# Kernel tuning notes

Hardware: AMD Instinct MI355X
Metric: run time of the kernel (lower is better)

## Reference

```python
import jax, jax.numpy as jnp
import numpy as np

N, E, D, K = 32768, 16384, 4, 8          # nodes, hyperedges, edges/node, nodes/edge
IN_DIM, OUT_DIM, EDGE_DIM, NUM_HEADS = 128, 128, 64, 8


def setup_inputs() -> dict:
    key = jax.random.key(0)
    ks = jax.random.split(key, 16)
    s_in = 1.0 / np.sqrt(IN_DIM)
    s_out = 1.0 / np.sqrt(OUT_DIM)
    s_edge = 1.0 / np.sqrt(EDGE_DIM)
    return {
        "x": jax.random.normal(ks[0], (N, IN_DIM), jnp.float32),
        "edge_attr": jax.random.normal(ks[1], (E, EDGE_DIM), jnp.float32),
        "node_edges": jax.random.randint(ks[2], (N, D), 0, E),   # hyperedges containing each node
        "edge_nodes": jax.random.randint(ks[3], (E, K), 0, N),   # nodes inside each hyperedge
        "W_lin": jax.random.normal(ks[4], (OUT_DIM, IN_DIM), jnp.float32) * s_in,
        "W_edge": jax.random.normal(ks[5], (OUT_DIM, EDGE_DIM), jnp.float32) * s_edge,
        "Wq": jax.random.normal(ks[6], (OUT_DIM, OUT_DIM), jnp.float32) * s_out,
        "Wk": jax.random.normal(ks[7], (OUT_DIM, OUT_DIM), jnp.float32) * s_out,
        "Wv": jax.random.normal(ks[8], (OUT_DIM, OUT_DIM), jnp.float32) * s_out,
        "bq": jnp.zeros((OUT_DIM,), jnp.float32),
        "bk": jnp.zeros((OUT_DIM,), jnp.float32),
        "bv": jnp.zeros((OUT_DIM,), jnp.float32),
        "Wo": jax.random.normal(ks[9], (OUT_DIM, OUT_DIM), jnp.float32) * s_out,
        "bo": jnp.zeros((OUT_DIM,), jnp.float32),
    }


def reference(x, edge_attr, node_edges, edge_nodes,
              W_lin, W_edge, Wq, Wk, Wv, bq, bk, bv, Wo, bo):
    n, out_dim = x.shape[0], W_lin.shape[0]
    hd = out_dim // NUM_HEADS
    L = node_edges.shape[1] * edge_nodes.shape[1]  # D*K keys per node

    Wh = x @ W_lin.T                               # [N, out]
    We = edge_attr @ W_edge.T                      # [E, out]

    u_idx = edge_nodes[node_edges]                 # [N, D, K] neighbor node ids
    vals = Wh[u_idx]                               # [N, D, K, out]
    keys = vals + We[node_edges][:, :, None, :]    # key = Wh[u] + We[e]
    keys = keys.reshape(n, L, out_dim)
    vals = vals.reshape(n, L, out_dim)

    # torch nn.MultiheadAttention: single query per node (query = Wh[v])
    q = (Wh @ Wq.T + bq).reshape(n, NUM_HEADS, hd)
    k = (keys @ Wk.T + bk).reshape(n, L, NUM_HEADS, hd)
    v = (vals @ Wv.T + bv).reshape(n, L, NUM_HEADS, hd)

    scores = jnp.einsum('nhd,nlhd->nhl', q, k) / jnp.sqrt(jnp.asarray(hd, q.dtype))
    attn = jax.nn.softmax(scores, axis=-1)         # [N, H, L]
    ctx = jnp.einsum('nhl,nlhd->nhd', attn, v).reshape(n, out_dim)
    out = ctx @ Wo.T + bo
    return jax.nn.relu(out)
```

## Files before the change

kernel.cpp:

```cpp
#include <hip/hip_runtime.h>

#define N_NODES 32768
#define N_EDGES 16384
#define DEG 4
#define KPE 8
#define DIM 128
#define EDIM 64

typedef float f32x4 __attribute__((ext_vector_type(4)));
typedef __bf16 bf16x8 __attribute__((ext_vector_type(8)));
typedef __bf16 bf16x2 __attribute__((ext_vector_type(2)));
typedef unsigned short u16x8 __attribute__((ext_vector_type(8)));
typedef unsigned int u32;
typedef unsigned int u32x4 __attribute__((ext_vector_type(4)));
typedef int i32x4 __attribute__((ext_vector_type(4)));

static __device__ __forceinline__ unsigned short f2bf(float f) {
  union { float f; unsigned int u; } v; v.f = f;
  unsigned int r = (v.u + 0x7FFFu + ((v.u >> 16) & 1u)) >> 16;
  return (unsigned short)r;
}
static __device__ __forceinline__ float bflo(unsigned int v) {
  union { unsigned int u; float f; } x; x.u = v << 16; return x.f;
}
static __device__ __forceinline__ float bfhi(unsigned int v) {
  union { unsigned int u; float f; } x; x.u = v & 0xffff0000u; return x.f;
}

#if __has_builtin(__builtin_amdgcn_fdot2_f32_bf16)
static __device__ __forceinline__ float dot2bf(unsigned int a, unsigned int b, float c) {
  return __builtin_amdgcn_fdot2_f32_bf16(
      __builtin_bit_cast(bf16x2, a), __builtin_bit_cast(bf16x2, b), c, false);
}
#else
static __device__ __forceinline__ float dot2bf(unsigned int a, unsigned int b, float c) {
  c = fmaf(bflo(a), bflo(b), c);
  return fmaf(bfhi(a), bfhi(b), c);
}
#endif

__global__ __launch_bounds__(256) void wprep_kernel(
    const float* __restrict__ Wq, const float* __restrict__ Wk,
    const float* __restrict__ Wv, const float* __restrict__ Wlin,
    const float* __restrict__ Wedge, const float* __restrict__ Wo,
    const int* __restrict__ node_edges, const int* __restrict__ enodes,
    unsigned short* __restrict__ CW, unsigned short* __restrict__ CWE,
    unsigned short* __restrict__ Wob, int* __restrict__ uidx)
{
  int id = blockIdx.x * 256 + threadIdx.x;
  if (id < 384 * 128) {
    int j = id >> 7, i = id & 127;
    const float* wrow; float scale = 1.0f;
    if (j < 128)      { wrow = Wq + j * 128; scale = 0.25f; }
    else if (j < 256) { wrow = Wk + (j - 128) * 128; }
    else              { wrow = Wv + (j - 256) * 128; }
    float s = 0.f;
    #pragma unroll 8
    for (int m = 0; m < 128; ++m) s += wrow[m] * Wlin[m * 128 + i];
    CW[id] = f2bf(s * scale);
  } else if (id < 384 * 128 + 128 * 64) {
    int id2 = id - 384 * 128; int j = id2 >> 6, t = id2 & 63;
    float s = 0.f;
    #pragma unroll 8
    for (int m = 0; m < 128; ++m) s += Wk[j * 128 + m] * Wedge[m * 64 + t];
    CWE[id2] = f2bf(s);
  } else if (id < 384 * 128 + 128 * 64 + 128 * 128) {
    int id3 = id - (384 * 128 + 128 * 64);
    Wob[id3] = f2bf(Wo[id3]);
  } else {
    int t = id - (384 * 128 + 128 * 64 + 128 * 128);
    int e = node_edges[t];
    i32x4 a = *(const i32x4*)(enodes + (size_t)e * KPE);
    i32x4 b = *(const i32x4*)(enodes + (size_t)e * KPE + 4);
    *(i32x4*)(uidx + (size_t)t * KPE)     = a;
    *(i32x4*)(uidx + (size_t)t * KPE + 4) = b;
  }
}

__global__ __launch_bounds__(256) void g12_kernel(
    const float* __restrict__ x, const unsigned short* __restrict__ CW,
    const float* __restrict__ bq, const float* __restrict__ bv,
    unsigned short* __restrict__ qb, unsigned short* __restrict__ Kb,
    unsigned short* __restrict__ Vb,
    const float* __restrict__ ea, const unsigned short* __restrict__ CWE,
    const float* __restrict__ bk, unsigned short* __restrict__ WeKb)
{
  const int wave = threadIdx.x >> 6, lane = threadIdx.x & 63;
  const int r16 = lane & 15, quad = lane >> 4;

  if (blockIdx.x < 512) {
    const int m0 = blockIdx.x * 64 + wave * 16;
    u16x8 av[4];
    const float* arow = x + (size_t)(m0 + r16) * DIM + quad * 8;
    #pragma unroll
    for (int kk = 0; kk < 4; ++kk) {
      float4 a0 = *(const float4*)(arow + kk * 32);
      float4 a1 = *(const float4*)(arow + kk * 32 + 4);
      u16x8 au;
      au[0] = f2bf(a0.x); au[1] = f2bf(a0.y); au[2] = f2bf(a0.z); au[3] = f2bf(a0.w);
      au[4] = f2bf(a1.x); au[5] = f2bf(a1.y); au[6] = f2bf(a1.z); au[7] = f2bf(a1.w);
      av[kk] = au;
    }
    #pragma unroll
    for (int g = 0; g < 6; ++g) {
      f32x4 acc[4];
      const f32x4 z = {0.f, 0.f, 0.f, 0.f};
      acc[0] = z; acc[1] = z; acc[2] = z; acc[3] = z;
      #pragma unroll
      for (int kk = 0; kk < 4; ++kk) {
        #pragma unroll
        for (int s = 0; s < 4; ++s) {
          u16x8 bu = *(const u16x8*)(CW + (size_t)(g * 64 + s * 16 + r16) * DIM + kk * 32 + quad * 8);
          acc[s] = __builtin_amdgcn_mfma_f32_16x16x32_bf16(
              __builtin_bit_cast(bf16x8, av[kk]), __builtin_bit_cast(bf16x8, bu), acc[s], 0, 0, 0);
        }
      }
      const int arr = g >> 1;
      const int colbase = (g & 1) * 64;
      unsigned short* dst = arr == 0 ? qb : (arr == 1 ? Kb : Vb);
      #pragma unroll
      for (int s = 0; s < 4; ++s) {
        int j = colbase + s * 16 + r16;
        float bias = arr == 0 ? 0.25f * bq[j] : (arr == 2 ? bv[j] : 0.f);
        #pragma unroll
        for (int r = 0; r < 4; ++r) {
          int m = m0 + quad * 4 + r;
          dst[(size_t)m * DIM + j] = f2bf(acc[s][r] + bias);
        }
      }
    }
  } else {
    const int idx = blockIdx.x - 512;
    const int m0 = (idx >> 1) * 64 + wave * 16;
    const int n0 = (idx & 1) * 64;
    f32x4 acc[4];
    const f32x4 z = {0.f, 0.f, 0.f, 0.f};
    acc[0] = z; acc[1] = z; acc[2] = z; acc[3] = z;
    const float* arow = ea + (size_t)(m0 + r16) * EDIM + quad * 8;
    #pragma unroll
    for (int kk = 0; kk < 2; ++kk) {
      float4 a0 = *(const float4*)(arow + kk * 32);
      float4 a1 = *(const float4*)(arow + kk * 32 + 4);
      u16x8 au;
      au[0] = f2bf(a0.x); au[1] = f2bf(a0.y); au[2] = f2bf(a0.z); au[3] = f2bf(a0.w);
      au[4] = f2bf(a1.x); au[5] = f2bf(a1.y); au[6] = f2bf(a1.z); au[7] = f2bf(a1.w);
      bf16x8 av = __builtin_bit_cast(bf16x8, au);
      #pragma unroll
      for (int s = 0; s < 4; ++s) {
        u16x8 bu = *(const u16x8*)(CWE + (size_t)(n0 + s * 16 + r16) * EDIM + kk * 32 + quad * 8);
        acc[s] = __builtin_amdgcn_mfma_f32_16x16x32_bf16(
            av, __builtin_bit_cast(bf16x8, bu), acc[s], 0, 0, 0);
      }
    }
    #pragma unroll
    for (int s = 0; s < 4; ++s) {
      int j = n0 + s * 16 + r16;
      float bias = bk[j];
      #pragma unroll
      for (int r = 0; r < 4; ++r) {
        int m = m0 + quad * 4 + r;
        WeKb[(size_t)m * DIM + j] = f2bf(acc[s][r] + bias);
      }
    }
  }
}

__global__ __launch_bounds__(64, 4) void attn_kernel(
    const unsigned short* __restrict__ qb, const unsigned short* __restrict__ Kb,
    const unsigned short* __restrict__ Vb, const unsigned short* __restrict__ WeKb,
    const int* __restrict__ nedges, const int* __restrict__ uidx,
    unsigned short* __restrict__ ctxb)
{
  __shared__ __align__(16) unsigned char ldsK[32 * 272];
  __shared__ __align__(16) unsigned char ldsE[4 * 272];
  __shared__ __align__(16) float ldsP[8][36];
  const int lane = threadIdx.x;
  const int n = blockIdx.x;
  const int l = lane & 31, half = lane >> 5;
  const int h = lane >> 3;
  const int c0 = lane * 2;

  const i32x4* up = (const i32x4*)(uidx + (size_t)n * 32);
  i32x4 m0 = __builtin_nontemporal_load(up + 0);
  i32x4 m1 = __builtin_nontemporal_load(up + 1);
  i32x4 m2 = __builtin_nontemporal_load(up + 2);
  i32x4 m3 = __builtin_nontemporal_load(up + 3);
  i32x4 m4 = __builtin_nontemporal_load(up + 4);
  i32x4 m5 = __builtin_nontemporal_load(up + 5);
  i32x4 m6 = __builtin_nontemporal_load(up + 6);
  i32x4 m7 = __builtin_nontemporal_load(up + 7);
  i32x4 e4 = __builtin_nontemporal_load((const i32x4*)(nedges + (size_t)n * DEG));

  const u32x4* qp = (const u32x4*)(qb + (size_t)n * DIM + half * 64);
  u32x4 qv[8];
  #pragma unroll
  for (int ch = 0; ch < 8; ++ch) qv[ch] = __builtin_nontemporal_load(qp + ch);

  asm volatile("" ::: "memory");

#define STAGE(ldsdst, table, row) do {                                          \
    const u32* gp_ = (const u32*)((table) + (size_t)(row) * DIM) + lane;        \
    __builtin_amdgcn_global_load_lds(                                           \
        (const __attribute__((address_space(1))) u32*)gp_,                      \
        (__attribute__((address_space(3))) u32*)(ldsdst), 4, 0, 0);             \
  } while (0)
  STAGE(ldsK + 0  * 272, Kb, m0.x); STAGE(ldsK + 1  * 272, Kb, m0.y);
  STAGE(ldsK + 2  * 272, Kb, m0.z); STAGE(ldsK + 3  * 272, Kb, m0.w);
  STAGE(ldsK + 4  * 272, Kb, m1.x); STAGE(ldsK + 5  * 272, Kb, m1.y);
  STAGE(ldsK + 6  * 272, Kb, m1.z); STAGE(ldsK + 7  * 272, Kb, m1.w);
  STAGE(ldsK + 8  * 272, Kb, m2.x); STAGE(ldsK + 9  * 272, Kb, m2.y);
  STAGE(ldsK + 10 * 272, Kb, m2.z); STAGE(ldsK + 11 * 272, Kb, m2.w);
  STAGE(ldsK + 12 * 272, Kb, m3.x); STAGE(ldsK + 13 * 272, Kb, m3.y);
  STAGE(ldsK + 14 * 272, Kb, m3.z); STAGE(ldsK + 15 * 272, Kb, m3.w);
  STAGE(ldsK + 16 * 272, Kb, m4.x); STAGE(ldsK + 17 * 272, Kb, m4.y);
  STAGE(ldsK + 18 * 272, Kb, m4.z); STAGE(ldsK + 19 * 272, Kb, m4.w);
  STAGE(ldsK + 20 * 272, Kb, m5.x); STAGE(ldsK + 21 * 272, Kb, m5.y);
  STAGE(ldsK + 22 * 272, Kb, m5.z); STAGE(ldsK + 23 * 272, Kb, m5.w);
  STAGE(ldsK + 24 * 272, Kb, m6.x); STAGE(ldsK + 25 * 272, Kb, m6.y);
  STAGE(ldsK + 26 * 272, Kb, m6.z); STAGE(ldsK + 27 * 272, Kb, m6.w);
  STAGE(ldsK + 28 * 272, Kb, m7.x); STAGE(ldsK + 29 * 272, Kb, m7.y);
  STAGE(ldsK + 30 * 272, Kb, m7.z); STAGE(ldsK + 31 * 272, Kb, m7.w);
  STAGE(ldsE + 0 * 272, WeKb, e4.x); STAGE(ldsE + 1 * 272, WeKb, e4.y);
  STAGE(ldsE + 2 * 272, WeKb, e4.z); STAGE(ldsE + 3 * 272, WeKb, e4.w);
#undef STAGE

  asm volatile("" ::: "memory");

  u32 vv[32];
#define VLOAD(t, row) vv[t] = *(const u32*)(Vb + (size_t)(row) * DIM + c0)
  VLOAD(0,  m0.x); VLOAD(1,  m0.y); VLOAD(2,  m0.z); VLOAD(3,  m0.w);
  VLOAD(4,  m1.x); VLOAD(5,  m1.y); VLOAD(6,  m1.z); VLOAD(7,  m1.w);
  VLOAD(8,  m2.x); VLOAD(9,  m2.y); VLOAD(10, m2.z); VLOAD(11, m2.w);
  VLOAD(12, m3.x); VLOAD(13, m3.y); VLOAD(14, m3.z); VLOAD(15, m3.w);
  VLOAD(16, m4.x); VLOAD(17, m4.y); VLOAD(18, m4.z); VLOAD(19, m4.w);
  VLOAD(20, m5.x); VLOAD(21, m5.y); VLOAD(22, m5.z); VLOAD(23, m5.w);
  VLOAD(24, m6.x); VLOAD(25, m6.y); VLOAD(26, m6.z); VLOAD(27, m6.w);
  VLOAD(28, m7.x); VLOAD(29, m7.y); VLOAD(30, m7.z); VLOAD(31, m7.w);
#undef VLOAD

  asm volatile("s_waitcnt vmcnt(32)" ::: "memory");

  const unsigned char* krow = ldsK + l * 272 + half * 128;
  const unsigned char* erow = ldsE + (l >> 3) * 272 + half * 128;
  float s[4] = {0.f, 0.f, 0.f, 0.f};
  #pragma unroll
  for (int ch = 0; ch < 8; ++ch) {
    uint4 kc = *(const uint4*)(krow + ch * 16);
    uint4 ec = *(const uint4*)(erow + ch * 16);
    const int hi = ch >> 1;
    float t = s[hi];
    t = dot2bf(qv[ch].x, kc.x, t); t = dot2bf(qv[ch].x, ec.x, t);
    t = dot2bf(qv[ch].y, kc.y, t); t = dot2bf(qv[ch].y, ec.y, t);
    t = dot2bf(qv[ch].z, kc.z, t); t = dot2bf(qv[ch].z, ec.z, t);
    t = dot2bf(qv[ch].w, kc.w, t); t = dot2bf(qv[ch].w, ec.w, t);
    s[hi] = t;
  }

  #pragma unroll
  for (int hi = 0; hi < 4; ++hi) {
    float vmax = s[hi];
    #pragma unroll
    for (int off = 16; off >= 1; off >>= 1)
      vmax = fmaxf(vmax, __shfl_xor(vmax, off, 32));
    float ex = __expf(s[hi] - vmax);
    float sum = ex;
    #pragma unroll
    for (int off = 16; off >= 1; off >>= 1)
      sum += __shfl_xor(sum, off, 32);
    ldsP[half * 4 + hi][l] = ex / sum;
  }

  float a0 = 0.f, a1 = 0.f;
  #pragma unroll
  for (int t = 0; t < 8; ++t) {
    float4 p4 = *(const float4*)&ldsP[h][t * 4];
    a0 = fmaf(p4.x, bflo(vv[t * 4 + 0]), a0); a1 = fmaf(p4.x, bfhi(vv[t * 4 + 0]), a1);
    a0 = fmaf(p4.y, bflo(vv[t * 4 + 1]), a0); a1 = fmaf(p4.y, bfhi(vv[t * 4 + 1]), a1);
    a0 = fmaf(p4.z, bflo(vv[t * 4 + 2]), a0); a1 = fmaf(p4.z, bfhi(vv[t * 4 + 2]), a1);
    a0 = fmaf(p4.w, bflo(vv[t * 4 + 3]), a0); a1 = fmaf(p4.w, bfhi(vv[t * 4 + 3]), a1);
  }
  unsigned int pk = (unsigned int)f2bf(a0) | ((unsigned int)f2bf(a1) << 16);
  __builtin_nontemporal_store(pk, (u32*)(ctxb + (size_t)n * DIM + c0));
}

__global__ __launch_bounds__(256) void g4_kernel(
    const unsigned short* __restrict__ ctxb, const unsigned short* __restrict__ Wob,
    const float* __restrict__ bo, float* __restrict__ out)
{
  const int wave = threadIdx.x >> 6, lane = threadIdx.x & 63;
  const int r16 = lane & 15, quad = lane >> 4;
  const int m0 = blockIdx.x * 64 + wave * 16;
  const int n0 = blockIdx.y * 64;

  f32x4 acc[4];
  const f32x4 z = {0.f, 0.f, 0.f, 0.f};
  acc[0] = z; acc[1] = z; acc[2] = z; acc[3] = z;

  #pragma unroll
  for (int kk = 0; kk < 4; ++kk) {
    u16x8 au = *(const u16x8*)(ctxb + (size_t)(m0 + r16) * DIM + kk * 32 + quad * 8);
    bf16x8 av = __builtin_bit_cast(bf16x8, au);
    #pragma unroll
    for (int s = 0; s < 4; ++s) {
      u16x8 bu = *(const u16x8*)(Wob + (size_t)(n0 + s * 16 + r16) * DIM + kk * 32 + quad * 8);
      acc[s] = __builtin_amdgcn_mfma_f32_16x16x32_bf16(
          av, __builtin_bit_cast(bf16x8, bu), acc[s], 0, 0, 0);
    }
  }

  #pragma unroll
  for (int s = 0; s < 4; ++s) {
    int j = n0 + s * 16 + r16;
    float bias = bo[j];
    #pragma unroll
    for (int r = 0; r < 4; ++r) {
      int m = m0 + quad * 4 + r;
      float v = acc[s][r] + bias;
      out[(size_t)m * DIM + j] = v > 0.f ? v : 0.f;
    }
  }
}

extern "C" void kernel_launch(void* const* d_in, const int* in_sizes, int n_in,
                              void* d_out, int out_size, void* d_ws, size_t ws_size,
                              hipStream_t stream)
{
  const float* x     = (const float*)d_in[0];
  const float* ea    = (const float*)d_in[1];
  const int* nedges  = (const int*)d_in[2];
  const int* enodes  = (const int*)d_in[3];
  const float* Wlin  = (const float*)d_in[4];
  const float* Wedge = (const float*)d_in[5];
  const float* Wq    = (const float*)d_in[6];
  const float* Wk    = (const float*)d_in[7];
  const float* Wv    = (const float*)d_in[8];
  const float* bq    = (const float*)d_in[9];
  const float* bk    = (const float*)d_in[10];
  const float* bv    = (const float*)d_in[11];
  const float* Wo    = (const float*)d_in[12];
  const float* bo    = (const float*)d_in[13];
  float* out = (float*)d_out;

  unsigned short* wsp = (unsigned short*)d_ws;
  unsigned short* CW   = wsp;  wsp += 384 * 128;
  unsigned short* CWE  = wsp;  wsp += 128 * 64;
  unsigned short* Wob  = wsp;  wsp += 128 * 128;
  unsigned short* qb   = wsp;  wsp += (size_t)N_NODES * DIM;
  unsigned short* Kb   = wsp;  wsp += (size_t)N_NODES * DIM;
  unsigned short* Vb   = wsp;  wsp += (size_t)N_NODES * DIM;
  unsigned short* WeKb = wsp;  wsp += (size_t)N_EDGES * DIM;
  unsigned short* ctxb = wsp;  wsp += (size_t)N_NODES * DIM;
  int* uidx = (int*)wsp;       wsp += (size_t)N_NODES * 32 * 2;

  wprep_kernel<<<dim3(800), dim3(256), 0, stream>>>(
      Wq, Wk, Wv, Wlin, Wedge, Wo, nedges, enodes, CW, CWE, Wob, uidx);
  g12_kernel<<<dim3(1024), dim3(256), 0, stream>>>(x, CW, bq, bv, qb, Kb, Vb, ea, CWE, bk, WeKb);
  attn_kernel<<<dim3(32768), dim3(64), 0, stream>>>(qb, Kb, Vb, WeKb, nedges, uidx, ctxb);
  g4_kernel<<<dim3(512, 2), dim3(256), 0, stream>>>(ctxb, Wob, bo, out);
}
```

Before: 205.2 us.

## Process two nodes per attention block with double-buffered LDS gather pipelining

Each attention workgroup now handles two nodes and double-buffers the K/edge LDS staging. The second node's index loads, K gathers and V loads are issued while the first node's scores and context are computed. The aim is to hide gather latency inside a single wave rather than relying only on occupancy. In exchange the block uses twice the LDS and more registers, the launch bound drops to 2 waves per SIMD, and the hand-tuned vmcnt counts must exactly match the issued loads.

```diff
diff --git a/kernel.cpp b/kernel.cpp
--- a/kernel.cpp
+++ b/kernel.cpp
@@ -165,122 +165,173 @@
   }
 }
 
-__global__ __launch_bounds__(64, 4) void attn_kernel(
+__global__ __launch_bounds__(64, 2) void attn_kernel(
     const unsigned short* __restrict__ qb, const unsigned short* __restrict__ Kb,
     const unsigned short* __restrict__ Vb, const unsigned short* __restrict__ WeKb,
     const int* __restrict__ nedges, const int* __restrict__ uidx,
     unsigned short* __restrict__ ctxb)
 {
-  __shared__ __align__(16) unsigned char ldsK[32 * 272];
-  __shared__ __align__(16) unsigned char ldsE[4 * 272];
-  __shared__ __align__(16) float ldsP[8][36];
+  __shared__ __align__(16) unsigned char ldsK[2][32 * 272];
+  __shared__ __align__(16) unsigned char ldsE[2][4 * 272];
+  __shared__ __align__(16) float ldsP[2][8][36];
   const int lane = threadIdx.x;
-  const int n = blockIdx.x;
   const int l = lane & 31, half = lane >> 5;
   const int h = lane >> 3;
   const int c0 = lane * 2;
-
-  const i32x4* up = (const i32x4*)(uidx + (size_t)n * 32);
-  i32x4 m0 = __builtin_nontemporal_load(up + 0);
-  i32x4 m1 = __builtin_nontemporal_load(up + 1);
-  i32x4 m2 = __builtin_nontemporal_load(up + 2);
-  i32x4 m3 = __builtin_nontemporal_load(up + 3);
-  i32x4 m4 = __builtin_nontemporal_load(up + 4);
-  i32x4 m5 = __builtin_nontemporal_load(up + 5);
-  i32x4 m6 = __builtin_nontemporal_load(up + 6);
-  i32x4 m7 = __builtin_nontemporal_load(up + 7);
-  i32x4 e4 = __builtin_nontemporal_load((const i32x4*)(nedges + (size_t)n * DEG));
-
-  const u32x4* qp = (const u32x4*)(qb + (size_t)n * DIM + half * 64);
-  u32x4 qv[8];
-  #pragma unroll
-  for (int ch = 0; ch < 8; ++ch) qv[ch] = __builtin_nontemporal_load(qp + ch);
-
-  asm volatile("" ::: "memory");
-
-#define STAGE(ldsdst, table, row) do {                                          \
+  const int nA = blockIdx.x * 2, nB = nA + 1;
+
+#define LOAD_IDX(mv, ev, node) do {                                             \
+    const i32x4* up_ = (const i32x4*)(uidx + (size_t)(node) * 32);              \
+    mv[0] = __builtin_nontemporal_load(up_ + 0);                                \
+    mv[1] = __builtin_nontemporal_load(up_ + 1);                                \
+    mv[2] = __builtin_nontemporal_load(up_ + 2);                                \
+    mv[3] = __builtin_nontemporal_load(up_ + 3);                                \
+    mv[4] = __builtin_nontemporal_load(up_ + 4);                                \
+    mv[5] = __builtin_nontemporal_load(up_ + 5);                                \
+    mv[6] = __builtin_nontemporal_load(up_ + 6);                                \
+    mv[7] = __builtin_nontemporal_load(up_ + 7);                                \
+    ev = __builtin_nontemporal_load((const i32x4*)(nedges + (size_t)(node) * DEG)); \
+  } while (0)
+
+#define STAGE1(ldsdst, table, row) do {                                         \
     const u32* gp_ = (const u32*)((table) + (size_t)(row) * DIM) + lane;        \
     __builtin_amdgcn_global_load_lds(                                           \
         (const __attribute__((address_space(1))) u32*)gp_,                      \
         (__attribute__((address_space(3))) u32*)(ldsdst), 4, 0, 0);             \
   } while (0)
-  STAGE(ldsK + 0  * 272, Kb, m0.x); STAGE(ldsK + 1  * 272, Kb, m0.y);
-  STAGE(ldsK + 2  * 272, Kb, m0.z); STAGE(ldsK + 3  * 272, Kb, m0.w);
-  STAGE(ldsK + 4  * 272, Kb, m1.x); STAGE(ldsK + 5  * 272, Kb, m1.y);
-  STAGE(ldsK + 6  * 272, Kb, m1.z); STAGE(ldsK + 7  * 272, Kb, m1.w);
-  STAGE(ldsK + 8  * 272, Kb, m2.x); STAGE(ldsK + 9  * 272, Kb, m2.y);
-  STAGE(ldsK + 10 * 272, Kb, m2.z); STAGE(ldsK + 11 * 272, Kb, m2.w);
-  STAGE(ldsK + 12 * 272, Kb, m3.x); STAGE(ldsK + 13 * 272, Kb, m3.y);
-  STAGE(ldsK + 14 * 272, Kb, m3.z); STAGE(ldsK + 15 * 272, Kb, m3.w);
-  STAGE(ldsK + 16 * 272, Kb, m4.x); STAGE(ldsK + 17 * 272, Kb, m4.y);
-  STAGE(ldsK + 18 * 272, Kb, m4.z); STAGE(ldsK + 19 * 272, Kb, m4.w);
-  STAGE(ldsK + 20 * 272, Kb, m5.x); STAGE(ldsK + 21 * 272, Kb, m5.y);
-  STAGE(ldsK + 22 * 272, Kb, m5.z); STAGE(ldsK + 23 * 272, Kb, m5.w);
-  STAGE(ldsK + 24 * 272, Kb, m6.x); STAGE(ldsK + 25 * 272, Kb, m6.y);
-  STAGE(ldsK + 26 * 272, Kb, m6.z); STAGE(ldsK + 27 * 272, Kb, m6.w);
-  STAGE(ldsK + 28 * 272, Kb, m7.x); STAGE(ldsK + 29 * 272, Kb, m7.y);
-  STAGE(ldsK + 30 * 272, Kb, m7.z); STAGE(ldsK + 31 * 272, Kb, m7.w);
-  STAGE(ldsE + 0 * 272, WeKb, e4.x); STAGE(ldsE + 1 * 272, WeKb, e4.y);
-  STAGE(ldsE + 2 * 272, WeKb, e4.z); STAGE(ldsE + 3 * 272, WeKb, e4.w);
-#undef STAGE
-
-  asm volatile("" ::: "memory");
-
-  u32 vv[32];
-#define VLOAD(t, row) vv[t] = *(const u32*)(Vb + (size_t)(row) * DIM + c0)
-  VLOAD(0,  m0.x); VLOAD(1,  m0.y); VLOAD(2,  m0.z); VLOAD(3,  m0.w);
-  VLOAD(4,  m1.x); VLOAD(5,  m1.y); VLOAD(6,  m1.z); VLOAD(7,  m1.w);
-  VLOAD(8,  m2.x); VLOAD(9,  m2.y); VLOAD(10, m2.z); VLOAD(11, m2.w);
-  VLOAD(12, m3.x); VLOAD(13, m3.y); VLOAD(14, m3.z); VLOAD(15, m3.w);
-  VLOAD(16, m4.x); VLOAD(17, m4.y); VLOAD(18, m4.z); VLOAD(19, m4.w);
-  VLOAD(20, m5.x); VLOAD(21, m5.y); VLOAD(22, m5.z); VLOAD(23, m5.w);
-  VLOAD(24, m6.x); VLOAD(25, m6.y); VLOAD(26, m6.z); VLOAD(27, m6.w);
-  VLOAD(28, m7.x); VLOAD(29, m7.y); VLOAD(30, m7.z); VLOAD(31, m7.w);
-#undef VLOAD
-
-  asm volatile("s_waitcnt vmcnt(32)" ::: "memory");
-
-  const unsigned char* krow = ldsK + l * 272 + half * 128;
-  const unsigned char* erow = ldsE + (l >> 3) * 272 + half * 128;
-  float s[4] = {0.f, 0.f, 0.f, 0.f};
-  #pragma unroll
-  for (int ch = 0; ch < 8; ++ch) {
-    uint4 kc = *(const uint4*)(krow + ch * 16);
-    uint4 ec = *(const uint4*)(erow + ch * 16);
-    const int hi = ch >> 1;
-    float t = s[hi];
-    t = dot2bf(qv[ch].x, kc.x, t); t = dot2bf(qv[ch].x, ec.x, t);
-    t = dot2bf(qv[ch].y, kc.y, t); t = dot2bf(qv[ch].y, ec.y, t);
-    t = dot2bf(qv[ch].z, kc.z, t); t = dot2bf(qv[ch].z, ec.z, t);
-    t = dot2bf(qv[ch].w, kc.w, t); t = dot2bf(qv[ch].w, ec.w, t);
-    s[hi] = t;
-  }
-
-  #pragma unroll
-  for (int hi = 0; hi < 4; ++hi) {
-    float vmax = s[hi];
-    #pragma unroll
-    for (int off = 16; off >= 1; off >>= 1)
-      vmax = fmaxf(vmax, __shfl_xor(vmax, off, 32));
-    float ex = __expf(s[hi] - vmax);
-    float sum = ex;
-    #pragma unroll
-    for (int off = 16; off >= 1; off >>= 1)
-      sum += __shfl_xor(sum, off, 32);
-    ldsP[half * 4 + hi][l] = ex / sum;
-  }
-
-  float a0 = 0.f, a1 = 0.f;
-  #pragma unroll
-  for (int t = 0; t < 8; ++t) {
-    float4 p4 = *(const float4*)&ldsP[h][t * 4];
-    a0 = fmaf(p4.x, bflo(vv[t * 4 + 0]), a0); a1 = fmaf(p4.x, bfhi(vv[t * 4 + 0]), a1);
-    a0 = fmaf(p4.y, bflo(vv[t * 4 + 1]), a0); a1 = fmaf(p4.y, bfhi(vv[t * 4 + 1]), a1);
-    a0 = fmaf(p4.z, bflo(vv[t * 4 + 2]), a0); a1 = fmaf(p4.z, bfhi(vv[t * 4 + 2]), a1);
-    a0 = fmaf(p4.w, bflo(vv[t * 4 + 3]), a0); a1 = fmaf(p4.w, bfhi(vv[t * 4 + 3]), a1);
-  }
-  unsigned int pk = (unsigned int)f2bf(a0) | ((unsigned int)f2bf(a1) << 16);
-  __builtin_nontemporal_store(pk, (u32*)(ctxb + (size_t)n * DIM + c0));
+
+#define STAGE_ALL(buf, mv, ev) do {                                             \
+    STAGE1(ldsK[buf] + 0  * 272, Kb, mv[0].x); STAGE1(ldsK[buf] + 1  * 272, Kb, mv[0].y); \
+    STAGE1(ldsK[buf] + 2  * 272, Kb, mv[0].z); STAGE1(ldsK[buf] + 3  * 272, Kb, mv[0].w); \
+    STAGE1(ldsK[buf] + 4  * 272, Kb, mv[1].x); STAGE1(ldsK[buf] + 5  * 272, Kb, mv[1].y); \
+    STAGE1(ldsK[buf] + 6  * 272, Kb, mv[1].z); STAGE1(ldsK[buf] + 7  * 272, Kb, mv[1].w); \
+    STAGE1(ldsK[buf] + 8  * 272, Kb, mv[2].x); STAGE1(ldsK[buf] + 9  * 272, Kb, mv[2].y); \
+    STAGE1(ldsK[buf] + 10 * 272, Kb, mv[2].z); STAGE1(ldsK[buf] + 11 * 272, Kb, mv[2].w); \
+    STAGE1(ldsK[buf] + 12 * 272, Kb, mv[3].x); STAGE1(ldsK[buf] + 13 * 272, Kb, mv[3].y); \
+    STAGE1(ldsK[buf] + 14 * 272, Kb, mv[3].z); STAGE1(ldsK[buf] + 15 * 272, Kb, mv[3].w); \
+    STAGE1(ldsK[buf] + 16 * 272, Kb, mv[4].x); STAGE1(ldsK[buf] + 17 * 272, Kb, mv[4].y); \
+    STAGE1(ldsK[buf] + 18 * 272, Kb, mv[4].z); STAGE1(ldsK[buf] + 19 * 272, Kb, mv[4].w); \
+    STAGE1(ldsK[buf] + 20 * 272, Kb, mv[5].x); STAGE1(ldsK[buf] + 21 * 272, Kb, mv[5].y); \
+    STAGE1(ldsK[buf] + 22 * 272, Kb, mv[5].z); STAGE1(ldsK[buf] + 23 * 272, Kb, mv[5].w); \
+    STAGE1(ldsK[buf] + 24 * 272, Kb, mv[6].x); STAGE1(ldsK[buf] + 25 * 272, Kb, mv[6].y); \
+    STAGE1(ldsK[buf] + 26 * 272, Kb, mv[6].z); STAGE1(ldsK[buf] + 27 * 272, Kb, mv[6].w); \
+    STAGE1(ldsK[buf] + 28 * 272, Kb, mv[7].x); STAGE1(ldsK[buf] + 29 * 272, Kb, mv[7].y); \
+    STAGE1(ldsK[buf] + 30 * 272, Kb, mv[7].z); STAGE1(ldsK[buf] + 31 * 272, Kb, mv[7].w); \
+    STAGE1(ldsE[buf] + 0 * 272, WeKb, ev.x); STAGE1(ldsE[buf] + 1 * 272, WeKb, ev.y); \
+    STAGE1(ldsE[buf] + 2 * 272, WeKb, ev.z); STAGE1(ldsE[buf] + 3 * 272, WeKb, ev.w); \
+  } while (0)
+
+#define LOAD_Q(qv, node) do {                                                   \
+    const u32x4* qp_ = (const u32x4*)(qb + (size_t)(node) * DIM + half * 64);   \
+    _Pragma("unroll")                                                           \
+    for (int ch = 0; ch < 8; ++ch) qv[ch] = __builtin_nontemporal_load(qp_ + ch); \
+  } while (0)
+
+#define VLOAD_ALL(vv, mv) do {                                                  \
+    _Pragma("unroll")                                                           \
+    for (int t_ = 0; t_ < 8; ++t_) {                                            \
+      vv[t_ * 4 + 0] = *(const u32*)(Vb + (size_t)mv[t_].x * DIM + c0);         \
+      vv[t_ * 4 + 1] = *(const u32*)(Vb + (size_t)mv[t_].y * DIM + c0);         \
+      vv[t_ * 4 + 2] = *(const u32*)(Vb + (size_t)mv[t_].z * DIM + c0);         \
+      vv[t_ * 4 + 3] = *(const u32*)(Vb + (size_t)mv[t_].w * DIM + c0);         \
+    }                                                                           \
+  } while (0)
+
+#define SCORE_SM(buf, qv) do {                                                  \
+    const unsigned char* krow_ = ldsK[buf] + l * 272 + half * 128;              \
+    const unsigned char* erow_ = ldsE[buf] + (l >> 3) * 272 + half * 128;       \
+    float s_[4] = {0.f, 0.f, 0.f, 0.f};                                         \
+    _Pragma("unroll")                                                           \
+    for (int ch = 0; ch < 8; ++ch) {                                            \
+      uint4 kc = *(const uint4*)(krow_ + ch * 16);                              \
+      uint4 ec = *(const uint4*)(erow_ + ch * 16);                              \
+      const int hi = ch >> 1;                                                   \
+      float t = s_[hi];                                                         \
+      t = dot2bf(qv[ch].x, kc.x, t); t = dot2bf(qv[ch].x, ec.x, t);             \
+      t = dot2bf(qv[ch].y, kc.y, t); t = dot2bf(qv[ch].y, ec.y, t);             \
+      t = dot2bf(qv[ch].z, kc.z, t); t = dot2bf(qv[ch].z, ec.z, t);             \
+      t = dot2bf(qv[ch].w, kc.w, t); t = dot2bf(qv[ch].w, ec.w, t);             \
+      s_[hi] = t;                                                               \
+    }                                                                           \
+    _Pragma("unroll")                                                           \
+    for (int hi = 0; hi < 4; ++hi) {                                            \
+      float vmax = s_[hi];                                                      \
+      _Pragma("unroll")                                                         \
+      for (int off = 16; off >= 1; off >>= 1)                                   \
+        vmax = fmaxf(vmax, __shfl_xor(vmax, off, 32));                          \
+      float ex = __expf(s_[hi] - vmax);                                         \
+      float sum = ex;                                                           \
+      _Pragma("unroll")                                                         \
+      for (int off = 16; off >= 1; off >>= 1)                                   \
+        sum += __shfl_xor(sum, off, 32);                                        \
+      ldsP[buf][half * 4 + hi][l] = ex / sum;                                   \
+    }                                                                           \
+  } while (0)
+
+#define CTX_COMPUTE(buf, vv, a0, a1) do {                                       \
+    a0 = 0.f; a1 = 0.f;                                                         \
+    _Pragma("unroll")                                                           \
+    for (int t_ = 0; t_ < 8; ++t_) {                                            \
+      float4 p4 = *(const float4*)&ldsP[buf][h][t_ * 4];                        \
+      a0 = fmaf(p4.x, bflo(vv[t_ * 4 + 0]), a0); a1 = fmaf(p4.x, bfhi(vv[t_ * 4 + 0]), a1); \
+      a0 = fmaf(p4.y, bflo(vv[t_ * 4 + 1]), a0); a1 = fmaf(p4.y, bfhi(vv[t_ * 4 + 1]), a1); \
+      a0 = fmaf(p4.z, bflo(vv[t_ * 4 + 2]), a0); a1 = fmaf(p4.z, bfhi(vv[t_ * 4 + 2]), a1); \
+      a0 = fmaf(p4.w, bflo(vv[t_ * 4 + 3]), a0); a1 = fmaf(p4.w, bfhi(vv[t_ * 4 + 3]), a1); \
+    }                                                                           \
+  } while (0)
+
+#define STORE_CTX(node, a0, a1) do {                                            \
+    unsigned int pk_ = (unsigned int)f2bf(a0) | ((unsigned int)f2bf(a1) << 16); \
+    __builtin_nontemporal_store(pk_, (u32*)(ctxb + (size_t)(node) * DIM + c0)); \
+  } while (0)
+
+  i32x4 mA[8], eA;
+  LOAD_IDX(mA, eA, nA);
+  asm volatile("" ::: "memory");
+  STAGE_ALL(0, mA, eA);
+  u32x4 qvA[8];
+  LOAD_Q(qvA, nA);
+  asm volatile("" ::: "memory");
+  u32 vvA[32];
+  VLOAD_ALL(vvA, mA);
+  i32x4 mB[8], eB;
+  LOAD_IDX(mB, eB, nB);
+  asm volatile("" ::: "memory");
+  asm volatile("s_waitcnt vmcnt(41)" ::: "memory");
+
+  SCORE_SM(0, qvA);
+
+  asm volatile("" ::: "memory");
+  asm volatile("s_waitcnt vmcnt(0)" ::: "memory");
+
+  STAGE_ALL(1, mB, eB);
+  u32x4 qvB[8];
+  LOAD_Q(qvB, nB);
+  asm volatile("" ::: "memory");
+
+  float a0A, a1A;
+  CTX_COMPUTE(0, vvA, a0A, a1A);
+  u32 vvB[32];
+  VLOAD_ALL(vvB, mB);
+  STORE_CTX(nA, a0A, a1A);
+
+  asm volatile("" ::: "memory");
+  asm volatile("s_waitcnt vmcnt(33)" ::: "memory");
+
+  SCORE_SM(1, qvB);
+
+  float a0B, a1B;
+  CTX_COMPUTE(1, vvB, a0B, a1B);
+  STORE_CTX(nB, a0B, a1B);
+
+#undef LOAD_IDX
+#undef STAGE1
+#undef STAGE_ALL
+#undef LOAD_Q
+#undef VLOAD_ALL
+#undef SCORE_SM
+#undef CTX_COMPUTE
+#undef STORE_CTX
 }
 
 __global__ __launch_bounds__(256) void g4_kernel(
@@ -355,6 +406,6 @@
   wprep_kernel<<<dim3(800), dim3(256), 0, stream>>>(
       Wq, Wk, Wv, Wlin, Wedge, Wo, nedges, enodes, CW, CWE, Wob, uidx);
   g12_kernel<<<dim3(1024), dim3(256), 0, stream>>>(x, CW, bq, bv, qb, Kb, Vb, ea, CWE, bk, WeKb);
-  attn_kernel<<<dim3(32768), dim3(64), 0, stream>>>(qb, Kb, Vb, WeKb, nedges, uidx, ctxb);
+  attn_kernel<<<dim3(16384), dim3(64), 0, stream>>>(qb, Kb, Vb, WeKb, nedges, uidx, ctxb);
   g4_kernel<<<dim3(512, 2), dim3(256), 0, stream>>>(ctxb, Wob, bo, out);
 }
```

After: 204.5 us. About the same (-0.3%).

## Precompute per-hyperedge key blocks so attention reads contiguous keys

Applied to the files above, without the earlier changes.

Adds a kernel that builds, for every hyperedge, its 8 key rows with the edge's key bias already added, stored contiguously in a new workspace buffer. The attention kernel then loads each lane's key row straight into registers from this buffer, replacing the scattered LDS-staged key gathers and the separate edge-bias dot products. This trades one extra kernel launch plus a 32 MB write and re-read for more coalesced key reads in attention, and adds a second bf16 rounding on the summed keys. The occupancy hint also drops from 4 to 3 blocks.

```diff
diff --git a/kernel.cpp b/kernel.cpp
--- a/kernel.cpp
+++ b/kernel.cpp
@@ -165,14 +165,39 @@
   }
 }
 
-__global__ __launch_bounds__(64, 4) void attn_kernel(
-    const unsigned short* __restrict__ qb, const unsigned short* __restrict__ Kb,
-    const unsigned short* __restrict__ Vb, const unsigned short* __restrict__ WeKb,
+__global__ __launch_bounds__(256) void g2b_kernel(
+    const unsigned short* __restrict__ Kb, const unsigned short* __restrict__ WeKb,
+    const int* __restrict__ enodes, unsigned short* __restrict__ Ke)
+{
+  const int wave = threadIdx.x >> 6, lane = threadIdx.x & 63;
+  const int e = blockIdx.x * 4 + wave;
+
+  const int* ep = enodes + (size_t)e * KPE;
+  i32x4 a = *(const i32x4*)ep;
+  i32x4 b = *(const i32x4*)(ep + 4);
+  u32 we = ((const u32*)(WeKb + (size_t)e * DIM))[lane];
+
+  int id[8] = {a.x, a.y, a.z, a.w, b.x, b.y, b.z, b.w};
+  u32 kr[8];
+  #pragma unroll
+  for (int t = 0; t < 8; ++t)
+    kr[t] = ((const u32*)(Kb + (size_t)id[t] * DIM))[lane];
+
+  const float wl = bflo(we), wh = bfhi(we);
+  u32* out = (u32*)(Ke + (size_t)e * KPE * DIM);
+  #pragma unroll
+  for (int t = 0; t < 8; ++t) {
+    u32 pk = (u32)f2bf(bflo(kr[t]) + wl) | ((u32)f2bf(bfhi(kr[t]) + wh) << 16);
+    out[t * (DIM / 2) + lane] = pk;
+  }
+}
+
+__global__ __launch_bounds__(64, 3) void attn_kernel(
+    const unsigned short* __restrict__ qb, const unsigned short* __restrict__ Ke,
+    const unsigned short* __restrict__ Vb,
     const int* __restrict__ nedges, const int* __restrict__ uidx,
     unsigned short* __restrict__ ctxb)
 {
-  __shared__ __align__(16) unsigned char ldsK[32 * 272];
-  __shared__ __align__(16) unsigned char ldsE[4 * 272];
   __shared__ __align__(16) float ldsP[8][36];
   const int lane = threadIdx.x;
   const int n = blockIdx.x;
@@ -180,6 +205,7 @@
   const int h = lane >> 3;
   const int c0 = lane * 2;
 
+  i32x4 e4 = __builtin_nontemporal_load((const i32x4*)(nedges + (size_t)n * DEG));
   const i32x4* up = (const i32x4*)(uidx + (size_t)n * 32);
   i32x4 m0 = __builtin_nontemporal_load(up + 0);
   i32x4 m1 = __builtin_nontemporal_load(up + 1);
@@ -189,7 +215,6 @@
   i32x4 m5 = __builtin_nontemporal_load(up + 5);
   i32x4 m6 = __builtin_nontemporal_load(up + 6);
   i32x4 m7 = __builtin_nontemporal_load(up + 7);
-  i32x4 e4 = __builtin_nontemporal_load((const i32x4*)(nedges + (size_t)n * DEG));
 
   const u32x4* qp = (const u32x4*)(qb + (size_t)n * DIM + half * 64);
   u32x4 qv[8];
@@ -198,31 +223,12 @@
 
   asm volatile("" ::: "memory");
 
-#define STAGE(ldsdst, table, row) do {                                          \
-    const u32* gp_ = (const u32*)((table) + (size_t)(row) * DIM) + lane;        \
-    __builtin_amdgcn_global_load_lds(                                           \
-        (const __attribute__((address_space(1))) u32*)gp_,                      \
-        (__attribute__((address_space(3))) u32*)(ldsdst), 4, 0, 0);             \
-  } while (0)
-  STAGE(ldsK + 0  * 272, Kb, m0.x); STAGE(ldsK + 1  * 272, Kb, m0.y);
-  STAGE(ldsK + 2  * 272, Kb, m0.z); STAGE(ldsK + 3  * 272, Kb, m0.w);
-  STAGE(ldsK + 4  * 272, Kb, m1.x); STAGE(ldsK + 5  * 272, Kb, m1.y);
-  STAGE(ldsK + 6  * 272, Kb, m1.z); STAGE(ldsK + 7  * 272, Kb, m1.w);
-  STAGE(ldsK + 8  * 272, Kb, m2.x); STAGE(ldsK + 9  * 272, Kb, m2.y);
-  STAGE(ldsK + 10 * 272, Kb, m2.z); STAGE(ldsK + 11 * 272, Kb, m2.w);
-  STAGE(ldsK + 12 * 272, Kb, m3.x); STAGE(ldsK + 13 * 272, Kb, m3.y);
-  STAGE(ldsK + 14 * 272, Kb, m3.z); STAGE(ldsK + 15 * 272, Kb, m3.w);
-  STAGE(ldsK + 16 * 272, Kb, m4.x); STAGE(ldsK + 17 * 272, Kb, m4.y);
-  STAGE(ldsK + 18 * 272, Kb, m4.z); STAGE(ldsK + 19 * 272, Kb, m4.w);
-  STAGE(ldsK + 20 * 272, Kb, m5.x); STAGE(ldsK + 21 * 272, Kb, m5.y);
-  STAGE(ldsK + 22 * 272, Kb, m5.z); STAGE(ldsK + 23 * 272, Kb, m5.w);
-  STAGE(ldsK + 24 * 272, Kb, m6.x); STAGE(ldsK + 25 * 272, Kb, m6.y);
-  STAGE(ldsK + 26 * 272, Kb, m6.z); STAGE(ldsK + 27 * 272, Kb, m6.w);
-  STAGE(ldsK + 28 * 272, Kb, m7.x); STAGE(ldsK + 29 * 272, Kb, m7.y);
-  STAGE(ldsK + 30 * 272, Kb, m7.z); STAGE(ldsK + 31 * 272, Kb, m7.w);
-  STAGE(ldsE + 0 * 272, WeKb, e4.x); STAGE(ldsE + 1 * 272, WeKb, e4.y);
-  STAGE(ldsE + 2 * 272, WeKb, e4.z); STAGE(ldsE + 3 * 272, WeKb, e4.w);
-#undef STAGE
+  const int d = l >> 3, kk = l & 7;
+  int el = d == 0 ? e4.x : (d == 1 ? e4.y : (d == 2 ? e4.z : e4.w));
+  const unsigned short* krow = Ke + ((size_t)el * KPE + kk) * DIM + half * 64;
+  u32x4 kc[8];
+  #pragma unroll
+  for (int ch = 0; ch < 8; ++ch) kc[ch] = *(const u32x4*)(krow + ch * 8);
 
   asm volatile("" ::: "memory");
 
@@ -238,21 +244,17 @@
   VLOAD(28, m7.x); VLOAD(29, m7.y); VLOAD(30, m7.z); VLOAD(31, m7.w);
 #undef VLOAD
 
-  asm volatile("s_waitcnt vmcnt(32)" ::: "memory");
-
-  const unsigned char* krow = ldsK + l * 272 + half * 128;
-  const unsigned char* erow = ldsE + (l >> 3) * 272 + half * 128;
+  asm volatile("" ::: "memory");
+
   float s[4] = {0.f, 0.f, 0.f, 0.f};
   #pragma unroll
   for (int ch = 0; ch < 8; ++ch) {
-    uint4 kc = *(const uint4*)(krow + ch * 16);
-    uint4 ec = *(const uint4*)(erow + ch * 16);
     const int hi = ch >> 1;
     float t = s[hi];
-    t = dot2bf(qv[ch].x, kc.x, t); t = dot2bf(qv[ch].x, ec.x, t);
-    t = dot2bf(qv[ch].y, kc.y, t); t = dot2bf(qv[ch].y, ec.y, t);
-    t = dot2bf(qv[ch].z, kc.z, t); t = dot2bf(qv[ch].z, ec.z, t);
-    t = dot2bf(qv[ch].w, kc.w, t); t = dot2bf(qv[ch].w, ec.w, t);
+    t = dot2bf(qv[ch].x, kc[ch].x, t);
+    t = dot2bf(qv[ch].y, kc[ch].y, t);
+    t = dot2bf(qv[ch].z, kc[ch].z, t);
+    t = dot2bf(qv[ch].w, kc[ch].w, t);
     s[hi] = t;
   }
 
@@ -351,10 +353,12 @@
   unsigned short* WeKb = wsp;  wsp += (size_t)N_EDGES * DIM;
   unsigned short* ctxb = wsp;  wsp += (size_t)N_NODES * DIM;
   int* uidx = (int*)wsp;       wsp += (size_t)N_NODES * 32 * 2;
+  unsigned short* Ke   = wsp;  wsp += (size_t)N_EDGES * KPE * DIM;
 
   wprep_kernel<<<dim3(800), dim3(256), 0, stream>>>(
       Wq, Wk, Wv, Wlin, Wedge, Wo, nedges, enodes, CW, CWE, Wob, uidx);
   g12_kernel<<<dim3(1024), dim3(256), 0, stream>>>(x, CW, bq, bv, qb, Kb, Vb, ea, CWE, bk, WeKb);
-  attn_kernel<<<dim3(32768), dim3(64), 0, stream>>>(qb, Kb, Vb, WeKb, nedges, uidx, ctxb);
+  g2b_kernel<<<dim3(N_EDGES / 4), dim3(256), 0, stream>>>(Kb, WeKb, enodes, Ke);
+  attn_kernel<<<dim3(32768), dim3(64), 0, stream>>>(qb, Ke, Vb, nedges, uidx, ctxb);
   g4_kernel<<<dim3(512, 2), dim3(256), 0, stream>>>(ctxb, Wob, bo, out);
 }
```

Result: slower. 219.6 us (+7.1%).
